# Optimization experiments

Hardware: AMD Instinct MI355X
Metric: run time of the kernel (lower is better)

## Reference

```python
import jax, jax.numpy as jnp
import numpy as np

NF = 64      # feature channels
DG = 8       # deformable groups
B, H, W = 4, 128, 128
K = 3        # kernel size
TAPS = K * K # 9 sampling taps per pixel per group


def _conv(x, w, b):
    # 3x3 stride-1 SAME conv, NCHW / OIHW
    y = jax.lax.conv_general_dilated(x, w, (1, 1), 'SAME',
                                     dimension_numbers=('NCHW', 'OIHW', 'NCHW'))
    return y + b[None, :, None, None]


def _lrelu(x):
    return jnp.where(x >= 0, x, 0.1 * x)


def _deform_conv(x, off_y, off_x, mask, w, b):
    """Modulated deformable conv v2 (3x3, stride 1, pad 1, dilation 1).
    x:     [B, C, H, W]
    off_y/off_x/mask: [B, dg, 9, H, W]
    w:     [Cout, C, 3, 3], b: [Cout]
    """
    Bn, C, Hn, Wn = x.shape
    dg = off_y.shape[1]
    cg = C // dg
    k = jnp.arange(K, dtype=x.dtype) - (K - 1) / 2  # [-1, 0, 1]
    ky = jnp.repeat(k, K)  # [9] row offsets
    kx = jnp.tile(k, K)    # [9] col offsets
    base_y = jnp.arange(Hn, dtype=x.dtype)[:, None]   # [H,1]
    base_x = jnp.arange(Wn, dtype=x.dtype)[None, :]   # [1,W]
    sy = off_y + ky[None, None, :, None, None] + base_y  # [B,dg,9,H,W]
    sx = off_x + kx[None, None, :, None, None] + base_x
    y0 = jnp.floor(sy)
    x0 = jnp.floor(sx)
    xg = x.reshape(Bn, dg, cg, Hn * Wn)
    val = jnp.zeros((Bn, dg, cg, TAPS, Hn, Wn), x.dtype)
    # bilinear interpolation over 4 corners, zero outside image
    for di in (0.0, 1.0):
        for dj in (0.0, 1.0):
            yi = y0 + di
            xi = x0 + dj
            wgt = (1.0 - jnp.abs(sy - yi)) * (1.0 - jnp.abs(sx - xi))
            valid = (yi >= 0) & (yi < Hn) & (xi >= 0) & (xi < Wn)
            idx = (jnp.clip(yi, 0, Hn - 1).astype(jnp.int32) * Wn
                   + jnp.clip(xi, 0, Wn - 1).astype(jnp.int32))  # [B,dg,9,H,W]
            g = jnp.take_along_axis(
                xg, idx.reshape(Bn, dg, 1, TAPS * Hn * Wn), axis=-1
            ).reshape(Bn, dg, cg, TAPS, Hn, Wn)
            val = val + (wgt * valid.astype(x.dtype))[:, :, None] * g
    val = val * mask[:, :, None]  # modulation
    out = jnp.einsum('bgckhw,ogck->bohw', val,
                     w.reshape(w.shape[0], dg, cg, TAPS))
    return out + b[None, :, None, None]


def setup_inputs() -> dict:
    key = jax.random.key(0)
    ks = jax.random.split(key, 12)
    s = lambda fan: 1.0 / np.sqrt(fan)
    return {
        'nbr': jax.random.normal(ks[0], (B, NF, H, W), jnp.float32),
        'ref': jax.random.normal(ks[1], (B, NF, H, W), jnp.float32),
        'w_off1': jax.random.normal(ks[2], (NF, 2 * NF, K, K), jnp.float32) * s(2 * NF * 9),
        'b_off1': jnp.zeros((NF,), jnp.float32),
        'w_off2': jax.random.normal(ks[3], (NF, NF, K, K), jnp.float32) * s(NF * 9),
        'b_off2': jnp.zeros((NF,), jnp.float32),
        # offset/mask conv: small init keeps sampled offsets modest (as trained DCNs do)
        'w_om': jax.random.normal(ks[4], (3 * DG * TAPS, NF, K, K), jnp.float32) * 0.01,
        'b_om': jnp.zeros((3 * DG * TAPS,), jnp.float32),
        'w_dcn': jax.random.normal(ks[5], (NF, NF, K, K), jnp.float32) * s(NF * 9),
        'b_dcn': jnp.zeros((NF,), jnp.float32),
    }


def reference(nbr, ref, w_off1, b_off1, w_off2, b_off2, w_om, b_om, w_dcn, b_dcn):
    off = _lrelu(_conv(jnp.concatenate([nbr, ref], axis=1), w_off1, b_off1))
    off = _lrelu(_conv(off, w_off2, b_off2))
    om = _conv(off, w_om, b_om)                 # [B, 3*dg*9, H, W]
    o1, o2, m = jnp.split(om, 3, axis=1)        # each [B, dg*9, H, W]
    Bn, _, Hn, Wn = nbr.shape
    off_y = o1.reshape(Bn, DG, TAPS, Hn, Wn)
    off_x = o2.reshape(Bn, DG, TAPS, Hn, Wn)
    mask = jax.nn.sigmoid(m).reshape(Bn, DG, TAPS, Hn, Wn)
    fea = _deform_conv(nbr, off_y, off_x, mask, w_dcn, b_dcn)
    return fea
```

## Files before the change

### kernel.cpp

```cpp
#include <hip/hip_runtime.h>
#include <hip/hip_bf16.h>
#include <math.h>

#define H_DIM 128
#define W_DIM 128
#define BATCH 4
#define HW (H_DIM * W_DIM)

typedef __attribute__((ext_vector_type(8))) short bf16x8;
typedef __attribute__((ext_vector_type(4))) float f32x4;
typedef __attribute__((ext_vector_type(4))) unsigned int u32x4;

static __device__ __forceinline__ unsigned short f2bf(float f) {
    __hip_bfloat16 h = __float2bfloat16(f);
    return *reinterpret_cast<unsigned short*>(&h);
}
static __device__ __forceinline__ float bf2f(unsigned short u) {
    return __uint_as_float(((unsigned int)u) << 16);
}

__global__ __launch_bounds__(256)
void prep_nhwc_kernel(const float* __restrict__ nbr, const float* __restrict__ ref,
                      unsigned short* __restrict__ dst,
                      unsigned short* __restrict__ gmaj) {
    __shared__ float s[128][65];
    const int b  = blockIdx.y;
    const int p0 = blockIdx.x * 64;
    const int t  = threadIdx.x;
    const int px = t & 63;
#pragma unroll
    for (int it = 0; it < 32; ++it) {
        int c = it * 4 + (t >> 6);
        const float* src = (c < 64) ? nbr : ref;
        int cs = c & 63;
        s[c][px] = src[(size_t)(b * 64 + cs) * HW + p0 + px];
    }
    __syncthreads();
#pragma unroll
    for (int it = 0; it < 4; ++it) {
        int idx = it * 256 + t;
        int p  = idx >> 4;
        int ut = idx & 15;
        int x  = (p0 + p) & 127;
        int key = (x + 1) & 7;
        int cpos = (ut & 8) | ((ut & 7) ^ key);
        bf16x8 v;
#pragma unroll
        for (int j = 0; j < 8; ++j)
            v[j] = (short)f2bf(s[ut * 8 + j][p]);
        *(bf16x8*)(dst + ((size_t)(b * HW + p0 + p) * 128 + cpos * 8)) = v;
    }
#pragma unroll
    for (int it = 0; it < 2; ++it) {
        int idx = it * 256 + t;
        int g   = idx >> 6;
        int p2  = idx & 63;
        bf16x8 v;
#pragma unroll
        for (int j = 0; j < 8; ++j)
            v[j] = (short)f2bf(s[g * 8 + j][p2]);
        *(bf16x8*)(gmaj + ((size_t)(b * 8 + g) * HW + p0 + p2) * 8) = v;
    }
}

__global__ void pack_all_kernel(const float* __restrict__ w1, const float* __restrict__ w2,
                                const float* __restrict__ wom, const float* __restrict__ wdcn,
                                unsigned short* __restrict__ wpk1, unsigned short* __restrict__ wpk2,
                                unsigned short* __restrict__ wpk3, unsigned short* __restrict__ wpkD) {
    int idx = blockIdx.x * 256 + threadIdx.x;
    const int N1 = 73728, N2 = 36864, N3 = 129024, N4 = 36864;
    const float* w; unsigned short* dst; int CIN, NCF, COUT;
    if (idx < N1)                { w = w1;   dst = wpk1; CIN = 128; NCF = 4;  COUT = 64; }
    else if (idx < N1+N2)        { idx -= N1;       w = w2;   dst = wpk2; CIN = 64; NCF = 4;  COUT = 64; }
    else if (idx < N1+N2+N3)     { idx -= N1+N2;    w = wom;  dst = wpk3; CIN = 64; NCF = 14; COUT = 216; }
    else if (idx < N1+N2+N3+N4)  { idx -= N1+N2+N3; w = wdcn; dst = wpkD; CIN = 64; NCF = 4;  COUT = 64; }
    else return;
    int j    = idx & 7;
    int lane = (idx >> 3) & 63;
    int frag = idx >> 9;
    int cf   = frag % NCF;
    int ks   = frag / NCF;
    int co = cf * 16 + (lane & 15);
    int k  = ks * 32 + (lane >> 4) * 8 + j;
    int t  = k / CIN;
    int ci = k % CIN;
    float v = (co < COUT) ? w[((size_t)co * CIN + ci) * 9 + t] : 0.f;
    dst[idx] = f2bf(v);
}

template<int CIN, int NKS, bool RELU>
__global__ __launch_bounds__(256, 3)
void conv64_mfma_kernel(const unsigned short* __restrict__ in,
                        const unsigned short* __restrict__ wpk,
                        const float* __restrict__ bias,
                        unsigned short* __restrict__ out)
{
    constexpr int ROWB = 66 * CIN * 2;
    __shared__ __align__(16) char smem[3 * ROWB];

    const int rb   = blockIdx.x;
    const int x0   = (rb & 1) * 64;
    const int y    = (rb >> 1) & 127;
    const int b    = rb >> 8;
    const int tid  = threadIdx.x;
    const int lane = tid & 63;
    const int wave = tid >> 6;
    const int l15  = lane & 15;
    const int q    = lane >> 4;
    const u32x4 zv = {0u, 0u, 0u, 0u};

    const int lstart = (x0 == 0) ? 1 : 0;
    const int lzero  = (x0 == 0) ? 0 : 65;
    for (int dy = 0; dy < 3; ++dy) {
        int yy = y + dy - 1;
        char* dstrow = smem + dy * ROWB;
        if (yy >= 0 && yy < H_DIM) {
            const char* src = (const char*)(in +
                ((size_t)(b * H_DIM + yy) * W_DIM + (x0 - 1 + lstart)) * CIN);
            for (int i = tid * 16; i < 65 * CIN * 2; i += 256 * 16)
                *(u32x4*)(dstrow + lstart * CIN * 2 + i) = *(const u32x4*)(src + i);
            if (tid < CIN / 8)
                *(u32x4*)(dstrow + lzero * CIN * 2 + tid * 16) = zv;
        } else {
            for (int i = tid * 16; i < 66 * CIN * 2; i += 256 * 16)
                *(u32x4*)(dstrow + i) = zv;
        }
    }
    __syncthreads();

    f32x4 acc[4];
#pragma unroll
    for (int pf = 0; pf < 4; ++pf)
        acc[pf] = (f32x4){0.f, 0.f, 0.f, 0.f};

#pragma unroll
    for (int ks = 0; ks < NKS; ++ks) {
        const int t   = ks / (CIN / 32);
        const int ci0 = (ks % (CIN / 32)) * 32;
        const int dy = t / 3, dx = t % 3;
        const int u  = (ci0 >> 3) + q;
        bf16x8 a[4];
#pragma unroll
        for (int pf = 0; pf < 4; ++pf) {
            const int l = pf * 16 + l15 + dx;
            const int upos = u ^ (l & 7);
            a[pf] = *(const bf16x8*)(smem + dy * ROWB + (l * CIN + upos * 8) * 2);
        }
        bf16x8 wfr = *(const bf16x8*)(wpk + ((size_t)(ks * 4 + wave) * 64 + lane) * 8);
#pragma unroll
        for (int pf = 0; pf < 4; ++pf)
            acc[pf] = __builtin_amdgcn_mfma_f32_16x16x32_bf16(a[pf], wfr, acc[pf], 0, 0, 0);
    }

    const int co = wave * 16 + l15;
    const float bv = bias[co];
#pragma unroll
    for (int pf = 0; pf < 4; ++pf)
#pragma unroll
        for (int r = 0; r < 4; ++r) {
            int x = x0 + pf * 16 + q * 4 + r;
            float v = acc[pf][r] + bv;
            if (RELU) v = (v >= 0.f) ? v : 0.1f * v;
            int cpos = (((co >> 3) ^ ((x + 1) & 7)) << 3) | (co & 7);
            out[((size_t)(b * H_DIM + y) * W_DIM + x) * 64 + cpos] = f2bf(v);
        }
}

struct GSlot {
    bf16x8 c00, c01, c10, c11;
    float w00, w01, w10, w11;
};

__global__ __launch_bounds__(256, 3)
void fused_om_deform_kernel(const unsigned short* __restrict__ in,
                            const unsigned short* __restrict__ xg,
                            const unsigned short* __restrict__ wpk3,
                            const unsigned short* __restrict__ wpkD,
                            const float* __restrict__ bom,
                            const float* __restrict__ bdcn,
                            float* __restrict__ out)
{
    constexpr int ROWB = 66 * 128;
    __shared__ __align__(16) char smem[216 * 72 * 2];
    unsigned short* om_lds = (unsigned short*)smem;

    const int hwid = blockIdx.x;
    const int rb   = (hwid & 7) * (BATCH * H_DIM * 2 / 8) + (hwid >> 3);
    const int x0   = (rb & 1) * 64;
    const int y    = (rb >> 1) & 127;
    const int b    = rb >> 8;
    const int tid  = threadIdx.x;
    const int lane = tid & 63;
    const int wave = tid >> 6;
    const int l15  = lane & 15;
    const int q    = lane >> 4;
    const u32x4 zv = {0u, 0u, 0u, 0u};

    const int lstart = (x0 == 0) ? 1 : 0;
    const int lzero  = (x0 == 0) ? 0 : 65;
    for (int dy = 0; dy < 3; ++dy) {
        int yy = y + dy - 1;
        char* dstrow = smem + dy * ROWB;
        if (yy >= 0 && yy < H_DIM) {
            const char* src = (const char*)(in +
                ((size_t)(b * H_DIM + yy) * W_DIM + (x0 - 1 + lstart)) * 64);
            for (int i = tid * 16; i < 65 * 128; i += 256 * 16)
                *(u32x4*)(dstrow + lstart * 128 + i) = *(const u32x4*)(src + i);
            if (tid < 8)
                *(u32x4*)(dstrow + lzero * 128 + tid * 16) = zv;
        } else {
            for (int i = tid * 16; i < 66 * 128; i += 256 * 16)
                *(u32x4*)(dstrow + i) = zv;
        }
    }
    __syncthreads();

    {
        f32x4 acc[4][4];
#pragma unroll
        for (int pf = 0; pf < 4; ++pf)
#pragma unroll
            for (int cfi = 0; cfi < 4; ++cfi)
                acc[pf][cfi] = (f32x4){0.f, 0.f, 0.f, 0.f};

#pragma unroll
        for (int ks = 0; ks < 18; ++ks) {
            const int t   = ks >> 1;
            const int ci0 = (ks & 1) * 32;
            const int dy = t / 3, dx = t % 3;
            bf16x8 a[4];
#pragma unroll
            for (int pf = 0; pf < 4; ++pf) {
                const int l = pf * 16 + l15 + dx;
                const int upos = ((ci0 >> 3) + q) ^ (l & 7);
                a[pf] = *(const bf16x8*)(smem + dy * ROWB + (l * 64 + upos * 8) * 2);
            }
#pragma unroll
            for (int cfi = 0; cfi < 4; ++cfi) {
                const int cf = wave + cfi * 4;
                if (cfi < 3 || wave < 2) {
                    bf16x8 wfr = *(const bf16x8*)(wpk3 + ((size_t)(ks * 14 + cf) * 64 + lane) * 8);
#pragma unroll
                    for (int pf = 0; pf < 4; ++pf)
                        acc[pf][cfi] = __builtin_amdgcn_mfma_f32_16x16x32_bf16(
                            a[pf], wfr, acc[pf][cfi], 0, 0, 0);
                }
            }
        }
        __syncthreads();

#pragma unroll
        for (int cfi = 0; cfi < 4; ++cfi) {
            const int cf = wave + cfi * 4;
            if (cfi < 3 || wave < 2) {
                const int co = cf * 16 + l15;
                if (co < 216) {
                    const float bv = bom[co];
#pragma unroll
                    for (int pf = 0; pf < 4; ++pf)
#pragma unroll
                        for (int r = 0; r < 4; ++r) {
                            int xl = pf * 16 + q * 4 + r;
                            om_lds[co * 72 + xl] = f2bf(acc[pf][cfi][r] + bv);
                        }
                }
            }
        }
    }
    __syncthreads();

    const int px0w = wave * 16;
    const int x    = x0 + px0w + l15;
    const int xl   = px0w + l15;

    f32x4 acc2[4];
#pragma unroll
    for (int cf = 0; cf < 4; ++cf)
        acc2[cf] = (f32x4){0.f, 0.f, 0.f, 0.f};

    auto OMLOAD = [&](int ks, float& oy, float& ox, float& mr) {
        const int och = ((ks & 1) * 4 + q) * 9 + (ks >> 1);
        oy = bf2f(om_lds[och * 72 + xl]);
        ox = bf2f(om_lds[(72 + och) * 72 + xl]);
        mr = bf2f(om_lds[(144 + och) * 72 + xl]);
    };

    auto GPREP = [&](int ks, float oy, float ox, float mr, GSlot& s) {
        const int tap = ks >> 1;
        const int g   = (ks & 1) * 4 + q;
        const int dy  = tap / 3 - 1;
        const int dx  = tap % 3 - 1;
        const float mask = 1.f / (1.f + __expf(-mr));

        const float sy = oy + (float)(dy + y);
        const float sx = ox + (float)(dx + x);
        const float fy = floorf(sy);
        const float fx = floorf(sx);
        const int y0  = (int)fy;
        const int xq0 = (int)fx;
        const float ay = sy - fy;
        const float ax = sx - fx;

        const bool vy0 = (y0 >= 0) && (y0 < H_DIM);
        const bool vy1 = (y0 >= -1) && (y0 < H_DIM - 1);
        const bool vx0 = (xq0 >= 0) && (xq0 < W_DIM);
        const bool vx1 = (xq0 >= -1) && (xq0 < W_DIM - 1);

        float w00 = (1.f - ay) * (1.f - ax); if (!(vy0 && vx0)) w00 = 0.f;
        float w01 = (1.f - ay) * ax;         if (!(vy0 && vx1)) w01 = 0.f;
        float w10 = ay * (1.f - ax);         if (!(vy1 && vx0)) w10 = 0.f;
        float w11 = ay * ax;                 if (!(vy1 && vx1)) w11 = 0.f;
        s.w00 = w00 * mask; s.w01 = w01 * mask;
        s.w10 = w10 * mask; s.w11 = w11 * mask;

        const int iy0 = min(max(y0, 0), H_DIM - 1);
        const int iy1 = min(max(y0 + 1, 0), H_DIM - 1);
        const int ix0 = min(max(xq0, 0), W_DIM - 1);
        const int ix1 = min(max(xq0 + 1, 0), W_DIM - 1);

        const unsigned short* gb = xg + (size_t)(b * 8 + g) * HW * 8;
        s.c00 = *(const bf16x8*)(gb + (size_t)(iy0 * W_DIM + ix0) * 8);
        s.c01 = *(const bf16x8*)(gb + (size_t)(iy0 * W_DIM + ix1) * 8);
        s.c10 = *(const bf16x8*)(gb + (size_t)(iy1 * W_DIM + ix0) * 8);
        s.c11 = *(const bf16x8*)(gb + (size_t)(iy1 * W_DIM + ix1) * 8);
    };

    auto CONSUME = [&](int ks, GSlot& s) {
        bf16x8 av;
#pragma unroll
        for (int j = 0; j < 8; ++j) {
            float v = s.w00 * bf2f((unsigned short)s.c00[j])
                    + s.w01 * bf2f((unsigned short)s.c01[j])
                    + s.w10 * bf2f((unsigned short)s.c10[j])
                    + s.w11 * bf2f((unsigned short)s.c11[j]);
            av[j] = (short)f2bf(v);
        }
#pragma unroll
        for (int cf = 0; cf < 4; ++cf) {
            bf16x8 wfr = *(const bf16x8*)(wpkD + ((size_t)(ks * 4 + cf) * 64 + lane) * 8);
            acc2[cf] = __builtin_amdgcn_mfma_f32_16x16x32_bf16(av, wfr, acc2[cf], 0, 0, 0);
        }
    };

    float oyA, oxA, mrA, oyB, oxB, mrB;
    GSlot GA, GB;
    OMLOAD(0, oyA, oxA, mrA);
    OMLOAD(1, oyB, oxB, mrB);
    GPREP(0, oyA, oxA, mrA, GA);
#pragma unroll
    for (int ks = 0; ks < 18; ks += 2) {
        if (ks + 2 < 18) OMLOAD(ks + 2, oyA, oxA, mrA);
        GPREP(ks + 1, oyB, oxB, mrB, GB);
        CONSUME(ks, GA);
        if (ks + 3 < 18) OMLOAD(ks + 3, oyB, oxB, mrB);
        if (ks + 2 < 18) GPREP(ks + 2, oyA, oxA, mrA, GA);
        CONSUME(ks + 1, GB);
    }

#pragma unroll
    for (int cf = 0; cf < 4; ++cf) {
        const int co = cf * 16 + l15;
        const float bv = bdcn[co];
#pragma unroll
        for (int r = 0; r < 4; ++r) {
            int xs = x0 + px0w + q * 4 + r;
            __builtin_nontemporal_store(acc2[cf][r] + bv,
                out + (size_t)(b * 64 + co) * HW + y * W_DIM + xs);
        }
    }
}

extern "C" void kernel_launch(void* const* d_in, const int* in_sizes, int n_in,
                              void* d_out, int out_size, void* d_ws, size_t ws_size,
                              hipStream_t stream) {
    const float* nbr  = (const float*)d_in[0];
    const float* ref  = (const float*)d_in[1];
    const float* w1   = (const float*)d_in[2];
    const float* b1   = (const float*)d_in[3];
    const float* w2   = (const float*)d_in[4];
    const float* b2   = (const float*)d_in[5];
    const float* wom  = (const float*)d_in[6];
    const float* bom  = (const float*)d_in[7];
    const float* wdcn = (const float*)d_in[8];
    const float* bdcn = (const float*)d_in[9];
    float* out = (float*)d_out;
    char* W = (char*)d_ws;

    unsigned short* in1  = (unsigned short*)(W + 0);
    unsigned short* c1o  = (unsigned short*)(W + 16777216);
    unsigned short* c2o  = (unsigned short*)(W + 25165824);
    unsigned short* nbrg = (unsigned short*)(W + 33554432);
    unsigned short* wpk1 = (unsigned short*)(W + 41943040);
    unsigned short* wpk2 = (unsigned short*)(W + 42090496);
    unsigned short* wpk3 = (unsigned short*)(W + 42164224);
    unsigned short* wpkD = (unsigned short*)(W + 42422272);

    prep_nhwc_kernel<<<dim3(HW / 64, BATCH), 256, 0, stream>>>(nbr, ref, in1, nbrg);
    pack_all_kernel<<<1080, 256, 0, stream>>>(w1, w2, wom, wdcn,
                                              wpk1, wpk2, wpk3, wpkD);

    conv64_mfma_kernel<128, 36, true>
        <<<dim3(BATCH * H_DIM * 2), 256, 0, stream>>>(in1, wpk1, b1, c1o);
    conv64_mfma_kernel<64, 18, true>
        <<<dim3(BATCH * H_DIM * 2), 256, 0, stream>>>(c1o, wpk2, b2, c2o);

    fused_om_deform_kernel<<<dim3(BATCH * H_DIM * 2), 256, 0, stream>>>(
        c2o, nbrg, wpk3, wpkD, bom, bdcn, out);
}
```

Measured before the change: 100.0 us.

## Halve fused deform tile width and split taps across waves with LDS reduction

The fused offset/deform kernel now processes 32-pixel row segments instead of 64, doubling the grid. In the deform phase, the K dimension (18 tap-group steps) is split between wave pairs, and partial accumulators are reduced through LDS before the store. LDS usage shrinks and the occupancy hint rises from 3 to 4 blocks per SM. This trades more parallelism and shorter per-wave gather chains against reloading the weight fragments and halo rows for more blocks, plus an extra barrier and reduction.

```diff
diff --git a/kernel.cpp b/kernel.cpp
--- a/kernel.cpp
+++ b/kernel.cpp
@@ -8,6 +8,7 @@
 #define HW (H_DIM * W_DIM)
 
 typedef __attribute__((ext_vector_type(8))) short bf16x8;
+typedef __attribute__((ext_vector_type(4))) short s16x4;
 typedef __attribute__((ext_vector_type(4))) float f32x4;
 typedef __attribute__((ext_vector_type(4))) unsigned int u32x4;
 
@@ -171,7 +172,7 @@
     float w00, w01, w10, w11;
 };
 
-__global__ __launch_bounds__(256, 3)
+__global__ __launch_bounds__(256, 4)
 void fused_om_deform_kernel(const unsigned short* __restrict__ in,
                             const unsigned short* __restrict__ xg,
                             const unsigned short* __restrict__ wpk3,
@@ -180,15 +181,17 @@
                             const float* __restrict__ bdcn,
                             float* __restrict__ out)
 {
-    constexpr int ROWB = 66 * 128;
-    __shared__ __align__(16) char smem[216 * 72 * 2];
+    constexpr int ROWB = 34 * 64 * 2;
+    constexpr int OMST = 48;
+    __shared__ __align__(16) char smem[216 * OMST * 2 + 2 * 64 * 20 * 4];
     unsigned short* om_lds = (unsigned short*)smem;
+    float* red = (float*)(smem + 216 * OMST * 2);
 
     const int hwid = blockIdx.x;
-    const int rb   = (hwid & 7) * (BATCH * H_DIM * 2 / 8) + (hwid >> 3);
-    const int x0   = (rb & 1) * 64;
-    const int y    = (rb >> 1) & 127;
-    const int b    = rb >> 8;
+    const int rb   = (hwid & 7) * (BATCH * H_DIM * 4 / 8) + (hwid >> 3);
+    const int x0   = (rb & 3) * 32;
+    const int y    = (rb >> 2) & 127;
+    const int b    = rb >> 9;
     const int tid  = threadIdx.x;
     const int lane = tid & 63;
     const int wave = tid >> 6;
@@ -196,29 +199,34 @@
     const int q    = lane >> 4;
     const u32x4 zv = {0u, 0u, 0u, 0u};
 
-    const int lstart = (x0 == 0) ? 1 : 0;
-    const int lzero  = (x0 == 0) ? 0 : 65;
-    for (int dy = 0; dy < 3; ++dy) {
-        int yy = y + dy - 1;
-        char* dstrow = smem + dy * ROWB;
-        if (yy >= 0 && yy < H_DIM) {
-            const char* src = (const char*)(in +
-                ((size_t)(b * H_DIM + yy) * W_DIM + (x0 - 1 + lstart)) * 64);
-            for (int i = tid * 16; i < 65 * 128; i += 256 * 16)
-                *(u32x4*)(dstrow + lstart * 128 + i) = *(const u32x4*)(src + i);
-            if (tid < 8)
-                *(u32x4*)(dstrow + lzero * 128 + tid * 16) = zv;
-        } else {
-            for (int i = tid * 16; i < 66 * 128; i += 256 * 16)
-                *(u32x4*)(dstrow + i) = zv;
+    {
+        const int c0 = (x0 == 0) ? 1 : 0;
+        const int c1 = (x0 == 96) ? 33 : 34;
+        const int nbytes = (c1 - c0) * 128;
+        for (int dy = 0; dy < 3; ++dy) {
+            int yy = y + dy - 1;
+            char* dstrow = smem + dy * ROWB;
+            if (yy >= 0 && yy < H_DIM) {
+                const char* src = (const char*)(in +
+                    ((size_t)(b * H_DIM + yy) * W_DIM + (x0 - 1 + c0)) * 64);
+                for (int i = tid * 16; i < nbytes; i += 256 * 16)
+                    *(u32x4*)(dstrow + c0 * 128 + i) = *(const u32x4*)(src + i);
+                if (x0 == 0 && tid < 8)
+                    *(u32x4*)(dstrow + 0 * 128 + tid * 16) = zv;
+                if (x0 == 96 && tid < 8)
+                    *(u32x4*)(dstrow + 33 * 128 + tid * 16) = zv;
+            } else {
+                for (int i = tid * 16; i < 34 * 128; i += 256 * 16)
+                    *(u32x4*)(dstrow + i) = zv;
+            }
         }
     }
     __syncthreads();
 
     {
-        f32x4 acc[4][4];
-#pragma unroll
-        for (int pf = 0; pf < 4; ++pf)
+        f32x4 acc[2][4];
+#pragma unroll
+        for (int pf = 0; pf < 2; ++pf)
 #pragma unroll
             for (int cfi = 0; cfi < 4; ++cfi)
                 acc[pf][cfi] = (f32x4){0.f, 0.f, 0.f, 0.f};
@@ -228,9 +236,9 @@
             const int t   = ks >> 1;
             const int ci0 = (ks & 1) * 32;
             const int dy = t / 3, dx = t % 3;
-            bf16x8 a[4];
-#pragma unroll
-            for (int pf = 0; pf < 4; ++pf) {
+            bf16x8 a[2];
+#pragma unroll
+            for (int pf = 0; pf < 2; ++pf) {
                 const int l = pf * 16 + l15 + dx;
                 const int upos = ((ci0 >> 3) + q) ^ (l & 7);
                 a[pf] = *(const bf16x8*)(smem + dy * ROWB + (l * 64 + upos * 8) * 2);
@@ -240,10 +248,8 @@
                 const int cf = wave + cfi * 4;
                 if (cfi < 3 || wave < 2) {
                     bf16x8 wfr = *(const bf16x8*)(wpk3 + ((size_t)(ks * 14 + cf) * 64 + lane) * 8);
-#pragma unroll
-                    for (int pf = 0; pf < 4; ++pf)
-                        acc[pf][cfi] = __builtin_amdgcn_mfma_f32_16x16x32_bf16(
-                            a[pf], wfr, acc[pf][cfi], 0, 0, 0);
+                    acc[0][cfi] = __builtin_amdgcn_mfma_f32_16x16x32_bf16(a[0], wfr, acc[0][cfi], 0, 0, 0);
+                    acc[1][cfi] = __builtin_amdgcn_mfma_f32_16x16x32_bf16(a[1], wfr, acc[1][cfi], 0, 0, 0);
                 }
             }
         }
@@ -257,35 +263,41 @@
                 if (co < 216) {
                     const float bv = bom[co];
 #pragma unroll
-                    for (int pf = 0; pf < 4; ++pf)
-#pragma unroll
-                        for (int r = 0; r < 4; ++r) {
-                            int xl = pf * 16 + q * 4 + r;
-                            om_lds[co * 72 + xl] = f2bf(acc[pf][cfi][r] + bv);
-                        }
+                    for (int pf = 0; pf < 2; ++pf) {
+                        s16x4 pk;
+#pragma unroll
+                        for (int r = 0; r < 4; ++r)
+                            pk[r] = (short)f2bf(acc[pf][cfi][r] + bv);
+                        *(s16x4*)(om_lds + co * OMST + pf * 16 + q * 4) = pk;
+                    }
                 }
             }
         }
     }
     __syncthreads();
 
-    const int px0w = wave * 16;
-    const int x    = x0 + px0w + l15;
-    const int xl   = px0w + l15;
+    const int pxgrp = wave >> 1;
+    const int khalf = wave & 1;
+    const int kbase = khalf * 9;
+    const int px0w  = pxgrp * 16;
+    const int xl    = px0w + l15;
+    const int x     = x0 + xl;
 
     f32x4 acc2[4];
 #pragma unroll
     for (int cf = 0; cf < 4; ++cf)
         acc2[cf] = (f32x4){0.f, 0.f, 0.f, 0.f};
 
-    auto OMLOAD = [&](int ks, float& oy, float& ox, float& mr) {
+    auto OMLOAD = [&](int i, float& oy, float& ox, float& mr) {
+        const int ks  = kbase + i;
         const int och = ((ks & 1) * 4 + q) * 9 + (ks >> 1);
-        oy = bf2f(om_lds[och * 72 + xl]);
-        ox = bf2f(om_lds[(72 + och) * 72 + xl]);
-        mr = bf2f(om_lds[(144 + och) * 72 + xl]);
+        oy = bf2f(om_lds[och * OMST + xl]);
+        ox = bf2f(om_lds[(72 + och) * OMST + xl]);
+        mr = bf2f(om_lds[(144 + och) * OMST + xl]);
     };
 
-    auto GPREP = [&](int ks, float oy, float ox, float mr, GSlot& s) {
+    auto GPREP = [&](int i, float oy, float ox, float mr, GSlot& s) {
+        const int ks  = kbase + i;
         const int tap = ks >> 1;
         const int g   = (ks & 1) * 4 + q;
         const int dy  = tap / 3 - 1;
@@ -325,7 +337,8 @@
         s.c11 = *(const bf16x8*)(gb + (size_t)(iy1 * W_DIM + ix1) * 8);
     };
 
-    auto CONSUME = [&](int ks, GSlot& s) {
+    auto CONSUME = [&](int i, GSlot& s) {
+        const int ks = kbase + i;
         bf16x8 av;
 #pragma unroll
         for (int j = 0; j < 8; ++j) {
@@ -342,30 +355,42 @@
         }
     };
 
-    float oyA, oxA, mrA, oyB, oxB, mrB;
-    GSlot GA, GB;
-    OMLOAD(0, oyA, oxA, mrA);
-    OMLOAD(1, oyB, oxB, mrB);
-    GPREP(0, oyA, oxA, mrA, GA);
-#pragma unroll
-    for (int ks = 0; ks < 18; ks += 2) {
-        if (ks + 2 < 18) OMLOAD(ks + 2, oyA, oxA, mrA);
-        GPREP(ks + 1, oyB, oxB, mrB, GB);
-        CONSUME(ks, GA);
-        if (ks + 3 < 18) OMLOAD(ks + 3, oyB, oxB, mrB);
-        if (ks + 2 < 18) GPREP(ks + 2, oyA, oxA, mrA, GA);
-        CONSUME(ks + 1, GB);
-    }
-
-#pragma unroll
-    for (int cf = 0; cf < 4; ++cf) {
-        const int co = cf * 16 + l15;
-        const float bv = bdcn[co];
-#pragma unroll
-        for (int r = 0; r < 4; ++r) {
-            int xs = x0 + px0w + q * 4 + r;
-            __builtin_nontemporal_store(acc2[cf][r] + bv,
-                out + (size_t)(b * 64 + co) * HW + y * W_DIM + xs);
+    {
+        float oyA, oxA, mrA, oyB, oxB, mrB;
+        GSlot GA, GB;
+        OMLOAD(0, oyA, oxA, mrA);
+        OMLOAD(1, oyB, oxB, mrB);
+        GPREP(0, oyA, oxA, mrA, GA);
+#pragma unroll
+        for (int i = 0; i < 8; i += 2) {
+            OMLOAD(i + 2, oyA, oxA, mrA);
+            GPREP(i + 1, oyB, oxB, mrB, GB);
+            CONSUME(i, GA);
+            if (i + 3 < 9) OMLOAD(i + 3, oyB, oxB, mrB);
+            GPREP(i + 2, oyA, oxA, mrA, GA);
+            CONSUME(i + 1, GB);
+        }
+        CONSUME(8, GA);
+    }
+
+    if (khalf == 1) {
+#pragma unroll
+        for (int cf = 0; cf < 4; ++cf)
+            *(f32x4*)&red[((size_t)pxgrp * 64 + lane) * 20 + cf * 4] = acc2[cf];
+    }
+    __syncthreads();
+    if (khalf == 0) {
+#pragma unroll
+        for (int cf = 0; cf < 4; ++cf) {
+            const f32x4 other = *(const f32x4*)&red[((size_t)pxgrp * 64 + lane) * 20 + cf * 4];
+            const int co = cf * 16 + l15;
+            const float bv = bdcn[co];
+#pragma unroll
+            for (int r = 0; r < 4; ++r) {
+                int xs = x0 + px0w + q * 4 + r;
+                __builtin_nontemporal_store(acc2[cf][r] + other[r] + bv,
+                    out + (size_t)(b * 64 + co) * HW + y * W_DIM + xs);
+            }
         }
     }
 }
@@ -404,6 +429,6 @@
     conv64_mfma_kernel<64, 18, true>
         <<<dim3(BATCH * H_DIM * 2), 256, 0, stream>>>(c1o, wpk2, b2, c2o);
 
-    fused_om_deform_kernel<<<dim3(BATCH * H_DIM * 2), 256, 0, stream>>>(
+    fused_om_deform_kernel<<<dim3(BATCH * H_DIM * 4), 256, 0, stream>>>(
         c2o, nbrg, wpk3, wpkD, bom, bdcn, out);
 }
```

Result: no change. 100.2 us (+0.2%).

## Stage deform gather neighborhood in LDS and use packed fp16 interpolation

Applied to the files above, without the earlier changes.

Preloads a 5x68 pixel, 8-group neighborhood of the group-major input into swizzled LDS. When every lane's offsets are under one pixel, the bilinear corner gathers read from this tile; otherwise they fall back to global loads. The gather input and DCN weights switch to fp16, so interpolation runs as packed half2 math feeding f16 MFMA. The explicit two-slot software pipeline is removed and the occupancy hint drops from 3 to 2 blocks per SM. The extra LDS and lower occupancy reduce latency hiding, and fp16 narrows the range of interpolated values.

```diff
diff --git a/kernel.cpp b/kernel.cpp
--- a/kernel.cpp
+++ b/kernel.cpp
@@ -8,8 +8,11 @@
 #define HW (H_DIM * W_DIM)
 
 typedef __attribute__((ext_vector_type(8))) short bf16x8;
+typedef __attribute__((ext_vector_type(4))) short s16x4;
 typedef __attribute__((ext_vector_type(4))) float f32x4;
 typedef __attribute__((ext_vector_type(4))) unsigned int u32x4;
+typedef _Float16 f16x2 __attribute__((ext_vector_type(2)));
+typedef _Float16 f16x8 __attribute__((ext_vector_type(8)));
 
 static __device__ __forceinline__ unsigned short f2bf(float f) {
     __hip_bfloat16 h = __float2bfloat16(f);
@@ -17,6 +20,10 @@
 }
 static __device__ __forceinline__ float bf2f(unsigned short u) {
     return __uint_as_float(((unsigned int)u) << 16);
+}
+static __device__ __forceinline__ unsigned short f2h(float f) {
+    _Float16 h = (_Float16)f;
+    return *reinterpret_cast<unsigned short*>(&h);
 }
 
 __global__ __launch_bounds__(256)
@@ -58,7 +65,7 @@
         bf16x8 v;
 #pragma unroll
         for (int j = 0; j < 8; ++j)
-            v[j] = (short)f2bf(s[g * 8 + j][p2]);
+            v[j] = (short)f2h(s[g * 8 + j][p2]);
         *(bf16x8*)(gmaj + ((size_t)(b * 8 + g) * HW + p0 + p2) * 8) = v;
     }
 }
@@ -69,11 +76,11 @@
                                 unsigned short* __restrict__ wpk3, unsigned short* __restrict__ wpkD) {
     int idx = blockIdx.x * 256 + threadIdx.x;
     const int N1 = 73728, N2 = 36864, N3 = 129024, N4 = 36864;
-    const float* w; unsigned short* dst; int CIN, NCF, COUT;
+    const float* w; unsigned short* dst; int CIN, NCF, COUT; bool asF16 = false;
     if (idx < N1)                { w = w1;   dst = wpk1; CIN = 128; NCF = 4;  COUT = 64; }
     else if (idx < N1+N2)        { idx -= N1;       w = w2;   dst = wpk2; CIN = 64; NCF = 4;  COUT = 64; }
     else if (idx < N1+N2+N3)     { idx -= N1+N2;    w = wom;  dst = wpk3; CIN = 64; NCF = 14; COUT = 216; }
-    else if (idx < N1+N2+N3+N4)  { idx -= N1+N2+N3; w = wdcn; dst = wpkD; CIN = 64; NCF = 4;  COUT = 64; }
+    else if (idx < N1+N2+N3+N4)  { idx -= N1+N2+N3; w = wdcn; dst = wpkD; CIN = 64; NCF = 4;  COUT = 64; asF16 = true; }
     else return;
     int j    = idx & 7;
     int lane = (idx >> 3) & 63;
@@ -85,7 +92,7 @@
     int t  = k / CIN;
     int ci = k % CIN;
     float v = (co < COUT) ? w[((size_t)co * CIN + ci) * 9 + t] : 0.f;
-    dst[idx] = f2bf(v);
+    dst[idx] = asF16 ? f2h(v) : f2bf(v);
 }
 
 template<int CIN, int NKS, bool RELU>
@@ -166,12 +173,7 @@
         }
 }
 
-struct GSlot {
-    bf16x8 c00, c01, c10, c11;
-    float w00, w01, w10, w11;
-};
-
-__global__ __launch_bounds__(256, 3)
+__global__ __launch_bounds__(256, 2)
 void fused_om_deform_kernel(const unsigned short* __restrict__ in,
                             const unsigned short* __restrict__ xg,
                             const unsigned short* __restrict__ wpk3,
@@ -181,8 +183,10 @@
                             float* __restrict__ out)
 {
     constexpr int ROWB = 66 * 128;
-    __shared__ __align__(16) char smem[216 * 72 * 2];
+    constexpr int OMB  = 216 * 72 * 2;
+    __shared__ __align__(16) char smem[OMB + 5 * 68 * 8 * 8 * 2];
     unsigned short* om_lds = (unsigned short*)smem;
+    unsigned short* tile   = (unsigned short*)(smem + OMB);
 
     const int hwid = blockIdx.x;
     const int rb   = (hwid & 7) * (BATCH * H_DIM * 2 / 8) + (hwid >> 3);
@@ -195,22 +199,38 @@
     const int l15  = lane & 15;
     const int q    = lane >> 4;
     const u32x4 zv = {0u, 0u, 0u, 0u};
-
-    const int lstart = (x0 == 0) ? 1 : 0;
-    const int lzero  = (x0 == 0) ? 0 : 65;
-    for (int dy = 0; dy < 3; ++dy) {
-        int yy = y + dy - 1;
-        char* dstrow = smem + dy * ROWB;
-        if (yy >= 0 && yy < H_DIM) {
-            const char* src = (const char*)(in +
-                ((size_t)(b * H_DIM + yy) * W_DIM + (x0 - 1 + lstart)) * 64);
-            for (int i = tid * 16; i < 65 * 128; i += 256 * 16)
-                *(u32x4*)(dstrow + lstart * 128 + i) = *(const u32x4*)(src + i);
-            if (tid < 8)
-                *(u32x4*)(dstrow + lzero * 128 + tid * 16) = zv;
-        } else {
-            for (int i = tid * 16; i < 66 * 128; i += 256 * 16)
-                *(u32x4*)(dstrow + i) = zv;
+    const int ty0  = y - 2;
+    const int tx0  = x0 - 2;
+
+    for (int i = tid; i < 5 * 8 * 68; i += 256) {
+        int col = i % 68;
+        int rg  = i / 68;
+        int g   = rg & 7;
+        int row = rg >> 3;
+        int gr = ty0 + row, gc = tx0 + col;
+        if (gr >= 0 && gr < H_DIM && gc >= 0 && gc < W_DIM) {
+            u32x4 v = *(const u32x4*)(xg + ((size_t)(b * 8 + g) * HW + gr * W_DIM + gc) * 8);
+            *(u32x4*)(tile + (((row * 68 + col) * 8) + (g ^ (gc & 7))) * 8) = v;
+        }
+    }
+
+    {
+        const int lstart = (x0 == 0) ? 1 : 0;
+        const int lzero  = (x0 == 0) ? 0 : 65;
+        for (int dy = 0; dy < 3; ++dy) {
+            int yy = y + dy - 1;
+            char* dstrow = smem + dy * ROWB;
+            if (yy >= 0 && yy < H_DIM) {
+                const char* src = (const char*)(in +
+                    ((size_t)(b * H_DIM + yy) * W_DIM + (x0 - 1 + lstart)) * 64);
+                for (int i = tid * 16; i < 65 * 128; i += 256 * 16)
+                    *(u32x4*)(dstrow + lstart * 128 + i) = *(const u32x4*)(src + i);
+                if (tid < 8)
+                    *(u32x4*)(dstrow + lzero * 128 + tid * 16) = zv;
+            } else {
+                for (int i = tid * 16; i < 66 * 128; i += 256 * 16)
+                    *(u32x4*)(dstrow + i) = zv;
+            }
         }
     }
     __syncthreads();
@@ -270,26 +290,25 @@
     __syncthreads();
 
     const int px0w = wave * 16;
-    const int x    = x0 + px0w + l15;
     const int xl   = px0w + l15;
+    const int x    = x0 + xl;
 
     f32x4 acc2[4];
 #pragma unroll
     for (int cf = 0; cf < 4; ++cf)
         acc2[cf] = (f32x4){0.f, 0.f, 0.f, 0.f};
 
-    auto OMLOAD = [&](int ks, float& oy, float& ox, float& mr) {
-        const int och = ((ks & 1) * 4 + q) * 9 + (ks >> 1);
-        oy = bf2f(om_lds[och * 72 + xl]);
-        ox = bf2f(om_lds[(72 + och) * 72 + xl]);
-        mr = bf2f(om_lds[(144 + och) * 72 + xl]);
-    };
-
-    auto GPREP = [&](int ks, float oy, float ox, float mr, GSlot& s) {
+#pragma unroll
+    for (int ks = 0; ks < 18; ++ks) {
         const int tap = ks >> 1;
         const int g   = (ks & 1) * 4 + q;
+        const int och = g * 9 + tap;
         const int dy  = tap / 3 - 1;
         const int dx  = tap % 3 - 1;
+
+        const float oy = bf2f(om_lds[och * 72 + xl]);
+        const float ox = bf2f(om_lds[(72 + och) * 72 + xl]);
+        const float mr = bf2f(om_lds[(144 + och) * 72 + xl]);
         const float mask = 1.f / (1.f + __expf(-mr));
 
         const float sy = oy + (float)(dy + y);
@@ -310,51 +329,52 @@
         float w01 = (1.f - ay) * ax;         if (!(vy0 && vx1)) w01 = 0.f;
         float w10 = ay * (1.f - ax);         if (!(vy1 && vx0)) w10 = 0.f;
         float w11 = ay * ax;                 if (!(vy1 && vx1)) w11 = 0.f;
-        s.w00 = w00 * mask; s.w01 = w01 * mask;
-        s.w10 = w10 * mask; s.w11 = w11 * mask;
+        w00 *= mask; w01 *= mask; w10 *= mask; w11 *= mask;
+        f16x2 h00, h01, h10, h11;
+        { _Float16 h = (_Float16)w00; h00 = (f16x2){h, h}; }
+        { _Float16 h = (_Float16)w01; h01 = (f16x2){h, h}; }
+        { _Float16 h = (_Float16)w10; h10 = (f16x2){h, h}; }
+        { _Float16 h = (_Float16)w11; h11 = (f16x2){h, h}; }
 
         const int iy0 = min(max(y0, 0), H_DIM - 1);
         const int iy1 = min(max(y0 + 1, 0), H_DIM - 1);
         const int ix0 = min(max(xq0, 0), W_DIM - 1);
         const int ix1 = min(max(xq0 + 1, 0), W_DIM - 1);
 
-        const unsigned short* gb = xg + (size_t)(b * 8 + g) * HW * 8;
-        s.c00 = *(const bf16x8*)(gb + (size_t)(iy0 * W_DIM + ix0) * 8);
-        s.c01 = *(const bf16x8*)(gb + (size_t)(iy0 * W_DIM + ix1) * 8);
-        s.c10 = *(const bf16x8*)(gb + (size_t)(iy1 * W_DIM + ix0) * 8);
-        s.c11 = *(const bf16x8*)(gb + (size_t)(iy1 * W_DIM + ix1) * 8);
-    };
-
-    auto CONSUME = [&](int ks, GSlot& s) {
-        bf16x8 av;
-#pragma unroll
-        for (int j = 0; j < 8; ++j) {
-            float v = s.w00 * bf2f((unsigned short)s.c00[j])
-                    + s.w01 * bf2f((unsigned short)s.c01[j])
-                    + s.w10 * bf2f((unsigned short)s.c10[j])
-                    + s.w11 * bf2f((unsigned short)s.c11[j]);
-            av[j] = (short)f2bf(v);
+        f16x8 c00, c01, c10, c11;
+        const bool inT = (fabsf(oy) < 1.0f) && (fabsf(ox) < 1.0f);
+        if (__all(inT)) {
+            const int r0 = (iy0 - ty0) * 68, r1 = (iy1 - ty0) * 68;
+            const int cA = ix0 - tx0, cB = ix1 - tx0;
+            const int uA = g ^ (ix0 & 7), uB = g ^ (ix1 & 7);
+            c00 = *(const f16x8*)(tile + ((r0 + cA) * 8 + uA) * 8);
+            c01 = *(const f16x8*)(tile + ((r0 + cB) * 8 + uB) * 8);
+            c10 = *(const f16x8*)(tile + ((r1 + cA) * 8 + uA) * 8);
+            c11 = *(const f16x8*)(tile + ((r1 + cB) * 8 + uB) * 8);
+        } else {
+            const unsigned short* gb = xg + (size_t)(b * 8 + g) * HW * 8;
+            c00 = *(const f16x8*)(gb + (size_t)(iy0 * W_DIM + ix0) * 8);
+            c01 = *(const f16x8*)(gb + (size_t)(iy0 * W_DIM + ix1) * 8);
+            c10 = *(const f16x8*)(gb + (size_t)(iy1 * W_DIM + ix0) * 8);
+            c11 = *(const f16x8*)(gb + (size_t)(iy1 * W_DIM + ix1) * 8);
+        }
+
+        f16x8 av;
+        {
+            const f16x2* p00 = reinterpret_cast<const f16x2*>(&c00);
+            const f16x2* p01 = reinterpret_cast<const f16x2*>(&c01);
+            const f16x2* p10 = reinterpret_cast<const f16x2*>(&c10);
+            const f16x2* p11 = reinterpret_cast<const f16x2*>(&c11);
+            f16x2* avp = reinterpret_cast<f16x2*>(&av);
+#pragma unroll
+            for (int j = 0; j < 4; ++j)
+                avp[j] = h00 * p00[j] + h01 * p01[j] + h10 * p10[j] + h11 * p11[j];
         }
 #pragma unroll
         for (int cf = 0; cf < 4; ++cf) {
-            bf16x8 wfr = *(const bf16x8*)(wpkD + ((size_t)(ks * 4 + cf) * 64 + lane) * 8);
-            acc2[cf] = __builtin_amdgcn_mfma_f32_16x16x32_bf16(av, wfr, acc2[cf], 0, 0, 0);
-        }
-    };
-
-    float oyA, oxA, mrA, oyB, oxB, mrB;
-    GSlot GA, GB;
-    OMLOAD(0, oyA, oxA, mrA);
-    OMLOAD(1, oyB, oxB, mrB);
-    GPREP(0, oyA, oxA, mrA, GA);
-#pragma unroll
-    for (int ks = 0; ks < 18; ks += 2) {
-        if (ks + 2 < 18) OMLOAD(ks + 2, oyA, oxA, mrA);
-        GPREP(ks + 1, oyB, oxB, mrB, GB);
-        CONSUME(ks, GA);
-        if (ks + 3 < 18) OMLOAD(ks + 3, oyB, oxB, mrB);
-        if (ks + 2 < 18) GPREP(ks + 2, oyA, oxA, mrA, GA);
-        CONSUME(ks + 1, GB);
+            f16x8 wfr = *(const f16x8*)(wpkD + ((size_t)(ks * 4 + cf) * 64 + lane) * 8);
+            acc2[cf] = __builtin_amdgcn_mfma_f32_16x16x32_f16(av, wfr, acc2[cf], 0, 0, 0);
+        }
     }
 
 #pragma unroll
```

Result: slower. 104.3 us (+4.3%).
